# Kernel tuning notes

Measured on AMD Instinct MI355X. Metric: run time of the kernel, lower is better.

## Reference

```python
import jax, jax.numpy as jnp
import numpy as np

N, E, G = 50000, 800000, 64
F_IN, H = 128, 256


def setup_inputs() -> dict:
    key = jax.random.key(0)
    ks = jax.random.split(key, 16)
    s = 0.05
    return {
        "x": jax.random.normal(ks[0], (N, F_IN), jnp.float32),
        "edge_index": jax.random.randint(ks[1], (2, E), 0, N, jnp.int32),
        "batch": jnp.sort(jax.random.randint(ks[2], (N,), 0, G, jnp.int32)),
        "W1": jax.random.normal(ks[3], (F_IN, H), jnp.float32) * s,
        "b1": jnp.zeros((H,), jnp.float32),
        "W2": jax.random.normal(ks[4], (H, H), jnp.float32) * s,
        "b2": jnp.zeros((H,), jnp.float32),
        "W3": jax.random.normal(ks[5], (H, H), jnp.float32) * s,
        "b3": jnp.zeros((H,), jnp.float32),
        "Wc1": jax.random.normal(ks[6], (2 * H, 512), jnp.float32) * s,
        "bc1": jnp.zeros((512,), jnp.float32),
        "Wc2": jax.random.normal(ks[7], (512, 256), jnp.float32) * s,
        "bc2": jnp.zeros((256,), jnp.float32),
        "Wc3": jax.random.normal(ks[8], (256, 5), jnp.float32) * s,
        "bc3": jnp.zeros((5,), jnp.float32),
    }


def _gcn_conv(x, src, dst, dis, W, b):
    # PyG GCNConv: h = x W; out = D^{-1/2}(A+I)D^{-1/2} h + b
    h = x @ W                                        # [N, H]
    coef = (dis[src] * dis[dst])[:, None]            # [E, 1]
    agg = jax.ops.segment_sum(h[src] * coef, dst, num_segments=x.shape[0])
    return agg + h * (dis * dis)[:, None] + b        # self-loop term


def reference(x, edge_index, batch, W1, b1, W2, b2, W3, b3,
              Wc1, bc1, Wc2, bc2, Wc3, bc3):
    src, dst = edge_index[0], edge_index[1]
    # degree with self loops (in-degree at dst, as PyG)
    deg = jax.ops.segment_sum(jnp.ones_like(dst, jnp.float32), dst,
                              num_segments=x.shape[0]) + 1.0
    dis = jax.lax.rsqrt(deg)                         # D^{-1/2}

    h = jax.nn.relu(_gcn_conv(x, src, dst, dis, W1, b1))  # dropout=identity (eval)
    h = jax.nn.relu(_gcn_conv(h, src, dst, dis, W2, b2))
    h = jax.nn.relu(_gcn_conv(h, src, dst, dis, W3, b3))

    # global mean / max pool per graph
    cnt = jax.ops.segment_sum(jnp.ones_like(batch, jnp.float32), batch,
                              num_segments=G)
    x_mean = jax.ops.segment_sum(h, batch, num_segments=G) / jnp.maximum(cnt, 1.0)[:, None]
    x_max = jax.ops.segment_max(h, batch, num_segments=G)
    x_max = jnp.where(cnt[:, None] > 0, x_max, 0.0)  # guard empty segments
    g = jnp.concatenate([x_mean, x_max], axis=1)     # [G, 512]

    g = jax.nn.relu(g @ Wc1 + bc1)
    g = jax.nn.relu(g @ Wc2 + bc2)
    return g @ Wc3 + bc3                             # [G, 5]
```

## Files before the change

kernel.cpp:

```cpp
#include <hip/hip_runtime.h>
#include <cstdint>

#define CDIV(a, b) (((a) + (b) - 1) / (b))

typedef short bf16x8 __attribute__((ext_vector_type(8)));
typedef float f32x4 __attribute__((ext_vector_type(4)));

__device__ inline ushort f2bf_rn(float f) {
    uint32_t u = __float_as_uint(f);
    uint32_t rounding = 0x7FFF + ((u >> 16) & 1);
    return (ushort)((u + rounding) >> 16);
}
__device__ inline float bf2f(ushort h) { return __uint_as_float((uint32_t)h << 16); }

__global__ void k_init(int* __restrict__ degc, int N, float* __restrict__ sumbuf,
                       int* __restrict__ maxbuf, int PB) {
    int i = blockIdx.x * blockDim.x + threadIdx.x;
    if (i < N) degc[i] = 0;
    if (i < PB) { sumbuf[i] = 0.f; maxbuf[i] = 0; }
}

__global__ void k_deg(const int* __restrict__ dst, int E, int* __restrict__ degc) {
    int e = blockIdx.x * blockDim.x + threadIdx.x;
    if (e < E) atomicAdd(&degc[dst[e]], 1);
}

__global__ void k_xsplit(const float* __restrict__ x, int n, ushort* __restrict__ xhi) {
    int i = blockIdx.x * blockDim.x + threadIdx.x;
    if (i < n) xhi[i] = f2bf_rn(x[i]);
}

__global__ void k_scan_partial(const int* __restrict__ degc, int N, int* __restrict__ csum) {
    __shared__ int sm[256];
    int t = threadIdx.x;
    int idx = blockIdx.x * 1024 + t * 4;
    int s = 0;
#pragma unroll
    for (int j = 0; j < 4; ++j)
        if (idx + j < N) s += degc[idx + j];
    sm[t] = s;
    __syncthreads();
    for (int off = 128; off > 0; off >>= 1) {
        if (t < off) sm[t] += sm[t + off];
        __syncthreads();
    }
    if (t == 0) csum[blockIdx.x] = sm[0];
}

__global__ void k_scan_chunks(const int* __restrict__ csum, int nch, int* __restrict__ coff,
                              int* __restrict__ row_ptr, int N, int E) {
    if (threadIdx.x == 0 && blockIdx.x == 0) {
        int run = 0;
        for (int i = 0; i < nch; ++i) { coff[i] = run; run += csum[i]; }
        row_ptr[N] = E;
    }
}

__global__ void k_scan_final(const int* __restrict__ degc, int N, const int* __restrict__ coff,
                             int* __restrict__ row_ptr, int* __restrict__ fill,
                             float* __restrict__ dis) {
    __shared__ int sm[256];
    int t = threadIdx.x;
    int idx = blockIdx.x * 1024 + t * 4;
    int v[4];
    int s = 0;
#pragma unroll
    for (int j = 0; j < 4; ++j) {
        v[j] = (idx + j < N) ? degc[idx + j] : 0;
        s += v[j];
    }
    sm[t] = s;
    __syncthreads();
    for (int off = 1; off < 256; off <<= 1) {
        int x = (t >= off) ? sm[t - off] : 0;
        __syncthreads();
        sm[t] += x;
        __syncthreads();
    }
    int excl = sm[t] - s + coff[blockIdx.x];
#pragma unroll
    for (int j = 0; j < 4; ++j) {
        if (idx + j < N) {
            row_ptr[idx + j] = excl;
            fill[idx + j] = 0;
            dis[idx + j] = rsqrtf((float)v[j] + 1.0f);
            excl += v[j];
        }
    }
}

__global__ void k_fill(const int* __restrict__ src, const int* __restrict__ dst, int E,
                       const int* __restrict__ row_ptr, int* __restrict__ fill,
                       int* __restrict__ esrc) {
    int e = blockIdx.x * blockDim.x + threadIdx.x;
    if (e >= E) return;
    int d = dst[e], s = src[e];
    int pos = row_ptr[d] + atomicAdd(&fill[d], 1);
    esrc[pos] = s;
}

template <int C, bool SELF_F32>
__global__ __launch_bounds__(256) void k_agg(const float* __restrict__ xf,
                                             const ushort* __restrict__ hhi,
                                             const float* __restrict__ dis,
                                             const int* __restrict__ row_ptr,
                                             const int* __restrict__ esrc, int N,
                                             ushort* __restrict__ ohi,
                                             ushort* __restrict__ olo) {
    constexpr int V = C / 64;
    int wave = (blockIdx.x * blockDim.x + threadIdx.x) >> 6;
    int lane = threadIdx.x & 63;
    if (wave >= N) return;
    const int i = wave;
    const float di = dis[i];
    const float dd = di * di;
    float acc[V];
    if constexpr (SELF_F32) {
        const float* xr = xf + (size_t)i * C + lane * V;
        if constexpr (V == 4) {
            float4 v = *reinterpret_cast<const float4*>(xr);
            acc[0] = dd * v.x; acc[1] = dd * v.y; acc[2] = dd * v.z; acc[3] = dd * v.w;
        } else {
            float2 v = *reinterpret_cast<const float2*>(xr);
            acc[0] = dd * v.x; acc[1] = dd * v.y;
        }
    } else {
        size_t sb = (size_t)i * C + lane * V;
        if constexpr (V == 4) {
            ushort4 h = *reinterpret_cast<const ushort4*>(hhi + sb);
            acc[0] = dd * bf2f(h.x); acc[1] = dd * bf2f(h.y);
            acc[2] = dd * bf2f(h.z); acc[3] = dd * bf2f(h.w);
        } else {
            ushort2 h = *reinterpret_cast<const ushort2*>(hhi + sb);
            acc[0] = dd * bf2f(h.x); acc[1] = dd * bf2f(h.y);
        }
    }
    const int p0 = row_ptr[i], p1 = row_ptr[i + 1];
    int p = p0;
    if constexpr (V == 4) {
        for (; p + 4 <= p1; p += 4) {
            int s0 = esrc[p], s1 = esrc[p + 1], s2 = esrc[p + 2], s3 = esrc[p + 3];
            float c0 = dis[s0] * di, c1 = dis[s1] * di, c2 = dis[s2] * di, c3 = dis[s3] * di;
            ushort4 v0 = *reinterpret_cast<const ushort4*>(hhi + (size_t)s0 * C + lane * V);
            ushort4 v1 = *reinterpret_cast<const ushort4*>(hhi + (size_t)s1 * C + lane * V);
            ushort4 v2 = *reinterpret_cast<const ushort4*>(hhi + (size_t)s2 * C + lane * V);
            ushort4 v3 = *reinterpret_cast<const ushort4*>(hhi + (size_t)s3 * C + lane * V);
            acc[0] += c0 * bf2f(v0.x); acc[1] += c0 * bf2f(v0.y);
            acc[2] += c0 * bf2f(v0.z); acc[3] += c0 * bf2f(v0.w);
            acc[0] += c1 * bf2f(v1.x); acc[1] += c1 * bf2f(v1.y);
            acc[2] += c1 * bf2f(v1.z); acc[3] += c1 * bf2f(v1.w);
            acc[0] += c2 * bf2f(v2.x); acc[1] += c2 * bf2f(v2.y);
            acc[2] += c2 * bf2f(v2.z); acc[3] += c2 * bf2f(v2.w);
            acc[0] += c3 * bf2f(v3.x); acc[1] += c3 * bf2f(v3.y);
            acc[2] += c3 * bf2f(v3.z); acc[3] += c3 * bf2f(v3.w);
        }
        for (; p < p1; ++p) {
            int s = esrc[p];
            float c = dis[s] * di;
            ushort4 v = *reinterpret_cast<const ushort4*>(hhi + (size_t)s * C + lane * V);
            acc[0] += c * bf2f(v.x); acc[1] += c * bf2f(v.y);
            acc[2] += c * bf2f(v.z); acc[3] += c * bf2f(v.w);
        }
    } else {
        for (; p + 4 <= p1; p += 4) {
            int s0 = esrc[p], s1 = esrc[p + 1], s2 = esrc[p + 2], s3 = esrc[p + 3];
            float c0 = dis[s0] * di, c1 = dis[s1] * di, c2 = dis[s2] * di, c3 = dis[s3] * di;
            ushort2 v0 = *reinterpret_cast<const ushort2*>(hhi + (size_t)s0 * C + lane * V);
            ushort2 v1 = *reinterpret_cast<const ushort2*>(hhi + (size_t)s1 * C + lane * V);
            ushort2 v2 = *reinterpret_cast<const ushort2*>(hhi + (size_t)s2 * C + lane * V);
            ushort2 v3 = *reinterpret_cast<const ushort2*>(hhi + (size_t)s3 * C + lane * V);
            acc[0] += c0 * bf2f(v0.x); acc[1] += c0 * bf2f(v0.y);
            acc[0] += c1 * bf2f(v1.x); acc[1] += c1 * bf2f(v1.y);
            acc[0] += c2 * bf2f(v2.x); acc[1] += c2 * bf2f(v2.y);
            acc[0] += c3 * bf2f(v3.x); acc[1] += c3 * bf2f(v3.y);
        }
        for (; p < p1; ++p) {
            int s = esrc[p];
            float c = dis[s] * di;
            ushort2 v = *reinterpret_cast<const ushort2*>(hhi + (size_t)s * C + lane * V);
            acc[0] += c * bf2f(v.x); acc[1] += c * bf2f(v.y);
        }
    }
    ushort hi[V], lo[V];
#pragma unroll
    for (int j = 0; j < V; ++j) {
        hi[j] = f2bf_rn(acc[j]);
        lo[j] = f2bf_rn(acc[j] - bf2f(hi[j]));
    }
    const int c0 = lane * V;
    size_t fb = ((size_t)(i >> 4) * (C / 32) + (c0 >> 5)) * 512 +
                (size_t)(((i & 15) + ((c0 >> 3) & 3) * 16) * 8 + (c0 & 7));
    if constexpr (V == 4) {
        *reinterpret_cast<ushort4*>(ohi + fb) = make_ushort4(hi[0], hi[1], hi[2], hi[3]);
        *reinterpret_cast<ushort4*>(olo + fb) = make_ushort4(lo[0], lo[1], lo[2], lo[3]);
    } else {
        *reinterpret_cast<ushort2*>(ohi + fb) = make_ushort2(hi[0], hi[1]);
        *reinterpret_cast<ushort2*>(olo + fb) = make_ushort2(lo[0], lo[1]);
    }
}

__global__ void k_wsplit(const float* __restrict__ W, int K, ushort* __restrict__ Whi,
                         ushort* __restrict__ Wlo) {
    int idx = blockIdx.x * 256 + threadIdx.x;
    if (idx >= K * 256) return;
    int k = idx >> 8, n = idx & 255;
    float v = W[idx];
    ushort hi = f2bf_rn(v);
    ushort lo = f2bf_rn(v - bf2f(hi));
    int ks = k >> 5, r = k & 31;
    int lane = (r >> 3) * 16 + (n & 15);
    int j = r & 7;
    size_t d = (((size_t)ks * 16 + (n >> 4)) * 64 + lane) * 8 + j;
    Whi[d] = hi;
    Wlo[d] = lo;
}

template <int K, bool POOL>
__global__ __launch_bounds__(256) void k_gemm_bf16(const ushort* __restrict__ Ahi,
                                                   const ushort* __restrict__ Alo,
                                                   const ushort* __restrict__ Whi,
                                                   const ushort* __restrict__ Wlo,
                                                   const float* __restrict__ bias, int M,
                                                   ushort* __restrict__ Hhi,
                                                   const int* __restrict__ batch,
                                                   float* __restrict__ sumbuf,
                                                   int* __restrict__ maxbuf) {
    __shared__ ushort Bs[2][2][8][512];
    const int t = threadIdx.x;
    const int w = t >> 6, lane = t & 63;
    constexpr int KS = K / 32;

    const int nwg = (int)gridDim.x;
    const int orig = (int)blockIdx.x;
    const int q = nwg >> 3, r = nwg & 7;
    const int xcd = orig & 7;
    const int swz = (xcd < r ? xcd * (q + 1) : r * (q + 1) + (xcd - r) * q) + (orig >> 3);
    const int bm = (swz >> 1) * 128;
    const int bn = (swz & 1) * 128;
    const int rw = bm + w * 32;

    f32x4 acc[2][8] = {};

    const size_t fbase = ((size_t)(rw >> 4) * KS) * 512 + (size_t)lane * 8;
    const ushort* pa_h = Ahi + fbase;
    const ushort* pa_l = Alo + fbase;
    const size_t rb1 = (size_t)KS * 512;
    const int nf0 = bn >> 4;

    bf16x8 sbh[2], sbl[2];
    auto loadB = [&](int ks) {
#pragma unroll
        for (int q2 = 0; q2 < 2; ++q2) {
            int nf = (w << 1) | q2;
            size_t widx = (((size_t)ks * 16 + nf0 + nf) * 64 + lane) * 8;
            sbh[q2] = *reinterpret_cast<const bf16x8*>(Whi + widx);
            sbl[q2] = *reinterpret_cast<const bf16x8*>(Wlo + widx);
        }
    };
    auto writeB = [&](int b) {
#pragma unroll
        for (int q2 = 0; q2 < 2; ++q2) {
            int nf = (w << 1) | q2;
            *reinterpret_cast<bf16x8*>(&Bs[b][0][nf][lane * 8]) = sbh[q2];
            *reinterpret_cast<bf16x8*>(&Bs[b][1][nf][lane * 8]) = sbl[q2];
        }
    };

    bf16x8 c0h, c0l, c1h, c1l, n0h, n0l, n1h, n1l, m0h, m0l, m1h, m1l;
    auto loadA = [&](int ks, bf16x8& x0h, bf16x8& x0l, bf16x8& x1h, bf16x8& x1l) {
        size_t o = (size_t)ks * 512;
        x0h = *reinterpret_cast<const bf16x8*>(pa_h + o);
        x0l = *reinterpret_cast<const bf16x8*>(pa_l + o);
        x1h = *reinterpret_cast<const bf16x8*>(pa_h + rb1 + o);
        x1l = *reinterpret_cast<const bf16x8*>(pa_l + rb1 + o);
    };

    loadB(0);
    writeB(0);
    loadA(0, c0h, c0l, c1h, c1l);
    if (KS > 1) loadA(1, n0h, n0l, n1h, n1l);
    if (KS > 1) loadB(1);
    __syncthreads();

#pragma unroll
    for (int ks = 0; ks < KS; ++ks) {
        const int buf = ks & 1;
        if (ks + 2 < KS) loadA(ks + 2, m0h, m0l, m1h, m1l);
#pragma unroll
        for (int nf = 0; nf < 8; ++nf) {
            bf16x8 bh = *reinterpret_cast<const bf16x8*>(&Bs[buf][0][nf][lane * 8]);
            bf16x8 bl = *reinterpret_cast<const bf16x8*>(&Bs[buf][1][nf][lane * 8]);
            acc[0][nf] = __builtin_amdgcn_mfma_f32_16x16x32_bf16(c0h, bh, acc[0][nf], 0, 0, 0);
            acc[0][nf] = __builtin_amdgcn_mfma_f32_16x16x32_bf16(c0h, bl, acc[0][nf], 0, 0, 0);
            acc[0][nf] = __builtin_amdgcn_mfma_f32_16x16x32_bf16(c0l, bh, acc[0][nf], 0, 0, 0);
            acc[1][nf] = __builtin_amdgcn_mfma_f32_16x16x32_bf16(c1h, bh, acc[1][nf], 0, 0, 0);
            acc[1][nf] = __builtin_amdgcn_mfma_f32_16x16x32_bf16(c1h, bl, acc[1][nf], 0, 0, 0);
            acc[1][nf] = __builtin_amdgcn_mfma_f32_16x16x32_bf16(c1l, bh, acc[1][nf], 0, 0, 0);
        }
        if (ks + 1 < KS) {
            writeB(buf ^ 1);
            if (ks + 2 < KS) loadB(ks + 2);
            __syncthreads();
            c0h = n0h; c0l = n0l; c1h = n1h; c1l = n1l;
            n0h = m0h; n0l = m0l; n1h = m1h; n1l = m1l;
        }
    }

    const int colq = lane & 15;
    const int rowq = (lane >> 4) * 4;

    if constexpr (!POOL) {
#pragma unroll
        for (int m = 0; m < 2; ++m) {
#pragma unroll
            for (int nf = 0; nf < 8; ++nf) {
                int col = bn + nf * 16 + colq;
                float bia = bias[col];
#pragma unroll
                for (int r2 = 0; r2 < 4; ++r2) {
                    int rr = rw + m * 16 + rowq + r2;
                    if (rr < M) {
                        float v = fmaxf(acc[m][nf][r2] + bia, 0.f);
                        Hhi[(size_t)rr * 256 + col] = f2bf_rn(v);
                    }
                }
            }
        }
    } else {
        int r0 = min(rw + rowq, M - 1);
        int r7 = min(rw + 16 + rowq + 3, M - 1);
        int g0 = batch[r0];
        int g7 = batch[r7];
        int gfirst = __shfl(g0, 0);
        bool uni = __all(g0 == gfirst && g7 == gfirst);
        if (uni) {
#pragma unroll
            for (int nf = 0; nf < 8; ++nf) {
                int col = bn + nf * 16 + colq;
                float bia = bias[col];
                float s = 0.f, mx = 0.f;
#pragma unroll
                for (int m = 0; m < 2; ++m) {
#pragma unroll
                    for (int r2 = 0; r2 < 4; ++r2) {
                        int rr = rw + m * 16 + rowq + r2;
                        float v = fmaxf(acc[m][nf][r2] + bia, 0.f);
                        if (rr < M) { s += v; mx = fmaxf(mx, v); }
                    }
                }
                s += __shfl_xor(s, 16);
                mx = fmaxf(mx, __shfl_xor(mx, 16));
                s += __shfl_xor(s, 32);
                mx = fmaxf(mx, __shfl_xor(mx, 32));
                if ((lane >> 4) == 0) {
                    atomicAdd(&sumbuf[gfirst * 256 + col], s);
                    atomicMax(&maxbuf[gfirst * 256 + col], __float_as_int(mx));
                }
            }
        } else {
#pragma unroll
            for (int nf = 0; nf < 8; ++nf) {
                int col = bn + nf * 16 + colq;
                float bia = bias[col];
#pragma unroll
                for (int m = 0; m < 2; ++m) {
#pragma unroll
                    for (int r2 = 0; r2 < 4; ++r2) {
                        int rr = rw + m * 16 + rowq + r2;
                        if (rr < M) {
                            float v = fmaxf(acc[m][nf][r2] + bia, 0.f);
                            int g = batch[rr];
                            atomicAdd(&sumbuf[g * 256 + col], v);
                            atomicMax(&maxbuf[g * 256 + col], __float_as_int(v));
                        }
                    }
                }
            }
        }
    }
}

__global__ __launch_bounds__(512) void k_head(const float* __restrict__ sumbuf,
                                              const int* __restrict__ maxbuf,
                                              const int* __restrict__ batch, int N,
                                              const float* __restrict__ Wc1,
                                              const float* __restrict__ bc1,
                                              const float* __restrict__ Wc2,
                                              const float* __restrict__ bc2,
                                              const float* __restrict__ Wc3,
                                              const float* __restrict__ bc3,
                                              float* __restrict__ out) {
    __shared__ float gf[512];
    __shared__ float h1[512];
    __shared__ float h2[256];
    __shared__ int cntS;
    const int g = blockIdx.x;
    const int t = threadIdx.x;

    if (t == 0) {
        int lo = 0, hi = N;
        while (lo < hi) { int mid = (lo + hi) >> 1; if (batch[mid] < g) lo = mid + 1; else hi = mid; }
        int s = lo;
        lo = 0; hi = N;
        while (lo < hi) { int mid = (lo + hi) >> 1; if (batch[mid] < g + 1) lo = mid + 1; else hi = mid; }
        cntS = lo - s;
    }
    __syncthreads();
    const int cnt = cntS;
    if (t < 256) {
        float mean = sumbuf[g * 256 + t] / fmaxf((float)cnt, 1.0f);
        float mx = __int_as_float(maxbuf[g * 256 + t]);
        if (cnt == 0) { mean = 0.f; mx = 0.f; }
        gf[t] = mean;
        gf[256 + t] = mx;
    }
    __syncthreads();
    {
        float a0 = 0.f, a1 = 0.f, a2 = 0.f, a3 = 0.f;
        for (int k = 0; k < 512; k += 4) {
            a0 += gf[k + 0] * Wc1[(size_t)(k + 0) * 512 + t];
            a1 += gf[k + 1] * Wc1[(size_t)(k + 1) * 512 + t];
            a2 += gf[k + 2] * Wc1[(size_t)(k + 2) * 512 + t];
            a3 += gf[k + 3] * Wc1[(size_t)(k + 3) * 512 + t];
        }
        h1[t] = fmaxf((a0 + a1) + (a2 + a3) + bc1[t], 0.f);
    }
    __syncthreads();
    if (t < 256) {
        float a0 = 0.f, a1 = 0.f, a2 = 0.f, a3 = 0.f;
        for (int k = 0; k < 512; k += 4) {
            a0 += h1[k + 0] * Wc2[(size_t)(k + 0) * 256 + t];
            a1 += h1[k + 1] * Wc2[(size_t)(k + 1) * 256 + t];
            a2 += h1[k + 2] * Wc2[(size_t)(k + 2) * 256 + t];
            a3 += h1[k + 3] * Wc2[(size_t)(k + 3) * 256 + t];
        }
        h2[t] = fmaxf((a0 + a1) + (a2 + a3) + bc2[t], 0.f);
    }
    __syncthreads();
    if (t < 5) {
        float a = bc3[t];
        for (int k = 0; k < 256; ++k) a += h2[k] * Wc3[(size_t)k * 5 + t];
        out[(size_t)g * 5 + t] = a;
    }
}

extern "C" void kernel_launch(void* const* d_in, const int* in_sizes, int n_in, void* d_out,
                              int out_size, void* d_ws, size_t ws_size, hipStream_t stream) {
    const float* x = (const float*)d_in[0];
    const int* eidx = (const int*)d_in[1];
    const int* batch = (const int*)d_in[2];
    const float* W1 = (const float*)d_in[3];
    const float* b1 = (const float*)d_in[4];
    const float* W2 = (const float*)d_in[5];
    const float* b2 = (const float*)d_in[6];
    const float* W3 = (const float*)d_in[7];
    const float* b3 = (const float*)d_in[8];
    const float* Wc1 = (const float*)d_in[9];
    const float* bc1 = (const float*)d_in[10];
    const float* Wc2 = (const float*)d_in[11];
    const float* bc2 = (const float*)d_in[12];
    const float* Wc3 = (const float*)d_in[13];
    const float* bc3 = (const float*)d_in[14];
    float* out = (float*)d_out;

    const int N = in_sizes[2];
    const int E = in_sizes[1] / 2;
    const int G = out_size / 5;
    const int* src = eidx;
    const int* dst = eidx + E;
    const int Npad = CDIV(N, 128) * 128;

    char* p = (char*)d_ws;
    auto alloc = [&](size_t bytes) {
        void* r = (void*)p;
        p += (bytes + 255) & ~(size_t)255;
        return r;
    };
    float* dis = (float*)alloc((size_t)N * 4);
    int* degc = (int*)alloc((size_t)N * 4);
    int* row_ptr = (int*)alloc((size_t)(N + 1) * 4);
    int* fill = (int*)alloc((size_t)N * 4);
    const int nch = CDIV(N, 1024);
    int* csum = (int*)alloc((size_t)nch * 4);
    int* coff = (int*)alloc((size_t)nch * 4);
    int* esrc = (int*)alloc((size_t)E * 4);
    float* sumbuf = (float*)alloc((size_t)G * 256 * 4);
    int* maxbuf = (int*)alloc((size_t)G * 256 * 4);
    ushort* Ahi = (ushort*)alloc((size_t)Npad * 256 * 2);
    ushort* Alo = (ushort*)alloc((size_t)Npad * 256 * 2);
    ushort* Hhi = (ushort*)alloc((size_t)N * 256 * 2);
    ushort* Xhi = (ushort*)alloc((size_t)N * 128 * 2);
    ushort* W1hi = (ushort*)alloc((size_t)128 * 256 * 2);
    ushort* W1lo = (ushort*)alloc((size_t)128 * 256 * 2);
    ushort* W2hi = (ushort*)alloc((size_t)256 * 256 * 2);
    ushort* W2lo = (ushort*)alloc((size_t)256 * 256 * 2);
    ushort* W3hi = (ushort*)alloc((size_t)256 * 256 * 2);
    ushort* W3lo = (ushort*)alloc((size_t)256 * 256 * 2);
    (void)ws_size;

    k_init<<<CDIV(N, 256), 256, 0, stream>>>(degc, N, sumbuf, maxbuf, G * 256);

    k_wsplit<<<CDIV(128 * 256, 256), 256, 0, stream>>>(W1, 128, W1hi, W1lo);
    k_wsplit<<<CDIV(256 * 256, 256), 256, 0, stream>>>(W2, 256, W2hi, W2lo);
    k_wsplit<<<CDIV(256 * 256, 256), 256, 0, stream>>>(W3, 256, W3hi, W3lo);
    k_xsplit<<<CDIV(N * 128, 256), 256, 0, stream>>>(x, N * 128, Xhi);

    k_deg<<<CDIV(E, 256), 256, 0, stream>>>(dst, E, degc);
    k_scan_partial<<<nch, 256, 0, stream>>>(degc, N, csum);
    k_scan_chunks<<<1, 64, 0, stream>>>(csum, nch, coff, row_ptr, N, E);
    k_scan_final<<<nch, 256, 0, stream>>>(degc, N, coff, row_ptr, fill, dis);
    k_fill<<<CDIV(E, 256), 256, 0, stream>>>(src, dst, E, row_ptr, fill, esrc);

    const int ggrid = CDIV(N, 128) * 2;

    k_agg<128, true><<<CDIV(N * 64, 256), 256, 0, stream>>>(x, Xhi, dis, row_ptr, esrc, N,
                                                            Ahi, Alo);
    k_gemm_bf16<128, false><<<ggrid, 256, 0, stream>>>(Ahi, Alo, W1hi, W1lo, b1, N, Hhi,
                                                       batch, sumbuf, maxbuf);
    k_agg<256, false><<<CDIV(N * 64, 256), 256, 0, stream>>>(nullptr, Hhi, dis, row_ptr,
                                                             esrc, N, Ahi, Alo);
    k_gemm_bf16<256, false><<<ggrid, 256, 0, stream>>>(Ahi, Alo, W2hi, W2lo, b2, N, Hhi,
                                                       batch, sumbuf, maxbuf);
    k_agg<256, false><<<CDIV(N * 64, 256), 256, 0, stream>>>(nullptr, Hhi, dis, row_ptr,
                                                             esrc, N, Ahi, Alo);
    k_gemm_bf16<256, true><<<ggrid, 256, 0, stream>>>(Ahi, Alo, W3hi, W3lo, b3, N, Hhi,
                                                      batch, sumbuf, maxbuf);

    k_head<<<G, 512, 0, stream>>>(sumbuf, maxbuf, batch, N, Wc1, bc1, Wc2, bc2, Wc3, bc3, out);
}
```

Measured before the change: 453.3 us.

## Drop LDS staging for B, stream weights directly into registers; row-major A

The GEMM no longer stages weight fragments through double-buffered shared memory with barriers. Each wave now loads its pre-swizzled B fragments straight from global memory into register arrays, prefetching a few slots ahead. The aggregation kernel writes A in plain row-major order instead of fragment-tiled order, and the GEMM reads A rows with per-lane row clamping, so padded buffers are no longer needed. This removes LDS traffic and barriers, but each wave now fetches all eight B fragments itself, which multiplies global/L2 weight reads by four and raises register pressure. The row-major A reads are also less contiguous per lane.

```diff
diff --git a/kernel.cpp b/kernel.cpp
--- a/kernel.cpp
+++ b/kernel.cpp
@@ -187,15 +187,13 @@
         hi[j] = f2bf_rn(acc[j]);
         lo[j] = f2bf_rn(acc[j] - bf2f(hi[j]));
     }
-    const int c0 = lane * V;
-    size_t fb = ((size_t)(i >> 4) * (C / 32) + (c0 >> 5)) * 512 +
-                (size_t)(((i & 15) + ((c0 >> 3) & 3) * 16) * 8 + (c0 & 7));
+    size_t ob = (size_t)i * C + lane * V;
     if constexpr (V == 4) {
-        *reinterpret_cast<ushort4*>(ohi + fb) = make_ushort4(hi[0], hi[1], hi[2], hi[3]);
-        *reinterpret_cast<ushort4*>(olo + fb) = make_ushort4(lo[0], lo[1], lo[2], lo[3]);
+        *reinterpret_cast<ushort4*>(ohi + ob) = make_ushort4(hi[0], hi[1], hi[2], hi[3]);
+        *reinterpret_cast<ushort4*>(olo + ob) = make_ushort4(lo[0], lo[1], lo[2], lo[3]);
     } else {
-        *reinterpret_cast<ushort2*>(ohi + fb) = make_ushort2(hi[0], hi[1]);
-        *reinterpret_cast<ushort2*>(olo + fb) = make_ushort2(lo[0], lo[1]);
+        *reinterpret_cast<ushort2*>(ohi + ob) = make_ushort2(hi[0], hi[1]);
+        *reinterpret_cast<ushort2*>(olo + ob) = make_ushort2(lo[0], lo[1]);
     }
 }
 
@@ -225,10 +223,11 @@
                                                    const int* __restrict__ batch,
                                                    float* __restrict__ sumbuf,
                                                    int* __restrict__ maxbuf) {
-    __shared__ ushort Bs[2][2][8][512];
     const int t = threadIdx.x;
     const int w = t >> 6, lane = t & 63;
     constexpr int KS = K / 32;
+    constexpr int NSLOT = KS * 8;
+    constexpr int DB = 4;
 
     const int nwg = (int)gridDim.x;
     const int orig = (int)blockIdx.x;
@@ -241,69 +240,48 @@
 
     f32x4 acc[2][8] = {};
 
-    const size_t fbase = ((size_t)(rw >> 4) * KS) * 512 + (size_t)lane * 8;
-    const ushort* pa_h = Ahi + fbase;
-    const ushort* pa_l = Alo + fbase;
-    const size_t rb1 = (size_t)KS * 512;
+    int row0 = min(rw + (lane & 15), M - 1);
+    int row1 = min(rw + 16 + (lane & 15), M - 1);
+    const int kbase = (lane >> 4) * 8;
+    const ushort* pa0h = Ahi + (size_t)row0 * K + kbase;
+    const ushort* pa0l = Alo + (size_t)row0 * K + kbase;
+    const ushort* pa1h = Ahi + (size_t)row1 * K + kbase;
+    const ushort* pa1l = Alo + (size_t)row1 * K + kbase;
     const int nf0 = bn >> 4;
-
-    bf16x8 sbh[2], sbl[2];
-    auto loadB = [&](int ks) {
-#pragma unroll
-        for (int q2 = 0; q2 < 2; ++q2) {
-            int nf = (w << 1) | q2;
-            size_t widx = (((size_t)ks * 16 + nf0 + nf) * 64 + lane) * 8;
-            sbh[q2] = *reinterpret_cast<const bf16x8*>(Whi + widx);
-            sbl[q2] = *reinterpret_cast<const bf16x8*>(Wlo + widx);
-        }
+    const size_t wlanep = (size_t)lane * 8;
+
+    bf16x8 BH[NSLOT], BL[NSLOT];
+    bf16x8 AH0[KS], AL0[KS], AH1[KS], AL1[KS];
+
+    auto loadBslot = [&](int u) {
+        const int ks = u >> 3, nf = u & 7;
+        size_t widx = (((size_t)ks * 16 + nf0 + nf) * 64) * 8 + wlanep;
+        BH[u] = *reinterpret_cast<const bf16x8*>(Whi + widx);
+        BL[u] = *reinterpret_cast<const bf16x8*>(Wlo + widx);
     };
-    auto writeB = [&](int b) {
-#pragma unroll
-        for (int q2 = 0; q2 < 2; ++q2) {
-            int nf = (w << 1) | q2;
-            *reinterpret_cast<bf16x8*>(&Bs[b][0][nf][lane * 8]) = sbh[q2];
-            *reinterpret_cast<bf16x8*>(&Bs[b][1][nf][lane * 8]) = sbl[q2];
-        }
+    auto loadAset = [&](int ks) {
+        AH0[ks] = *reinterpret_cast<const bf16x8*>(pa0h + ks * 32);
+        AL0[ks] = *reinterpret_cast<const bf16x8*>(pa0l + ks * 32);
+        AH1[ks] = *reinterpret_cast<const bf16x8*>(pa1h + ks * 32);
+        AL1[ks] = *reinterpret_cast<const bf16x8*>(pa1l + ks * 32);
     };
 
-    bf16x8 c0h, c0l, c1h, c1l, n0h, n0l, n1h, n1l, m0h, m0l, m1h, m1l;
-    auto loadA = [&](int ks, bf16x8& x0h, bf16x8& x0l, bf16x8& x1h, bf16x8& x1l) {
-        size_t o = (size_t)ks * 512;
-        x0h = *reinterpret_cast<const bf16x8*>(pa_h + o);
-        x0l = *reinterpret_cast<const bf16x8*>(pa_l + o);
-        x1h = *reinterpret_cast<const bf16x8*>(pa_h + rb1 + o);
-        x1l = *reinterpret_cast<const bf16x8*>(pa_l + rb1 + o);
-    };
-
-    loadB(0);
-    writeB(0);
-    loadA(0, c0h, c0l, c1h, c1l);
-    if (KS > 1) loadA(1, n0h, n0l, n1h, n1l);
-    if (KS > 1) loadB(1);
-    __syncthreads();
-
-#pragma unroll
-    for (int ks = 0; ks < KS; ++ks) {
-        const int buf = ks & 1;
-        if (ks + 2 < KS) loadA(ks + 2, m0h, m0l, m1h, m1l);
-#pragma unroll
-        for (int nf = 0; nf < 8; ++nf) {
-            bf16x8 bh = *reinterpret_cast<const bf16x8*>(&Bs[buf][0][nf][lane * 8]);
-            bf16x8 bl = *reinterpret_cast<const bf16x8*>(&Bs[buf][1][nf][lane * 8]);
-            acc[0][nf] = __builtin_amdgcn_mfma_f32_16x16x32_bf16(c0h, bh, acc[0][nf], 0, 0, 0);
-            acc[0][nf] = __builtin_amdgcn_mfma_f32_16x16x32_bf16(c0h, bl, acc[0][nf], 0, 0, 0);
-            acc[0][nf] = __builtin_amdgcn_mfma_f32_16x16x32_bf16(c0l, bh, acc[0][nf], 0, 0, 0);
-            acc[1][nf] = __builtin_amdgcn_mfma_f32_16x16x32_bf16(c1h, bh, acc[1][nf], 0, 0, 0);
-            acc[1][nf] = __builtin_amdgcn_mfma_f32_16x16x32_bf16(c1h, bl, acc[1][nf], 0, 0, 0);
-            acc[1][nf] = __builtin_amdgcn_mfma_f32_16x16x32_bf16(c1l, bh, acc[1][nf], 0, 0, 0);
-        }
-        if (ks + 1 < KS) {
-            writeB(buf ^ 1);
-            if (ks + 2 < KS) loadB(ks + 2);
-            __syncthreads();
-            c0h = n0h; c0l = n0l; c1h = n1h; c1l = n1l;
-            n0h = m0h; n0l = m0l; n1h = m1h; n1l = m1l;
-        }
+#pragma unroll
+    for (int u = 0; u < DB; ++u) loadBslot(u);
+    loadAset(0);
+    if (KS > 1) loadAset(1);
+
+#pragma unroll
+    for (int u = 0; u < NSLOT; ++u) {
+        const int ks = u >> 3, nf = u & 7;
+        if (u + DB < NSLOT) loadBslot(u + DB);
+        if (nf == 0 && ks + 2 < KS) loadAset(ks + 2);
+        acc[0][nf] = __builtin_amdgcn_mfma_f32_16x16x32_bf16(AH0[ks], BH[u], acc[0][nf], 0, 0, 0);
+        acc[0][nf] = __builtin_amdgcn_mfma_f32_16x16x32_bf16(AH0[ks], BL[u], acc[0][nf], 0, 0, 0);
+        acc[0][nf] = __builtin_amdgcn_mfma_f32_16x16x32_bf16(AL0[ks], BH[u], acc[0][nf], 0, 0, 0);
+        acc[1][nf] = __builtin_amdgcn_mfma_f32_16x16x32_bf16(AH1[ks], BH[u], acc[1][nf], 0, 0, 0);
+        acc[1][nf] = __builtin_amdgcn_mfma_f32_16x16x32_bf16(AH1[ks], BL[u], acc[1][nf], 0, 0, 0);
+        acc[1][nf] = __builtin_amdgcn_mfma_f32_16x16x32_bf16(AL1[ks], BH[u], acc[1][nf], 0, 0, 0);
     }
 
     const int colq = lane & 15;
@@ -468,7 +446,6 @@
     const int G = out_size / 5;
     const int* src = eidx;
     const int* dst = eidx + E;
-    const int Npad = CDIV(N, 128) * 128;
 
     char* p = (char*)d_ws;
     auto alloc = [&](size_t bytes) {
@@ -486,8 +463,8 @@
     int* esrc = (int*)alloc((size_t)E * 4);
     float* sumbuf = (float*)alloc((size_t)G * 256 * 4);
     int* maxbuf = (int*)alloc((size_t)G * 256 * 4);
-    ushort* Ahi = (ushort*)alloc((size_t)Npad * 256 * 2);
-    ushort* Alo = (ushort*)alloc((size_t)Npad * 256 * 2);
+    ushort* Ahi = (ushort*)alloc((size_t)N * 256 * 2);
+    ushort* Alo = (ushort*)alloc((size_t)N * 256 * 2);
     ushort* Hhi = (ushort*)alloc((size_t)N * 256 * 2);
     ushort* Xhi = (ushort*)alloc((size_t)N * 128 * 2);
     ushort* W1hi = (ushort*)alloc((size_t)128 * 256 * 2);
```

Result: slower. 473.7 us (+4.5%).

## Use row-major A layout and 64-row GEMM tiles with one M-fragment per wave

Applied to the files above, without the earlier changes.

The aggregation kernel now writes its hi/lo bf16 outputs in plain row-major order instead of a pre-swizzled MFMA fragment layout. The GEMM reads A directly from row-major rows, with each lane loading 8 contiguous bf16. GEMM block tiles shrink from 128 to 64 rows, so each wave handles 16 rows, and the grid doubles. The intent is simpler, more coalesced scatter-free writes in aggregation and more GEMM blocks for occupancy. The cost is that the W fragments in LDS are reused over half as many rows, and the A loads become strided row reads.

```diff
diff --git a/kernel.cpp b/kernel.cpp
--- a/kernel.cpp
+++ b/kernel.cpp
@@ -187,15 +187,13 @@
         hi[j] = f2bf_rn(acc[j]);
         lo[j] = f2bf_rn(acc[j] - bf2f(hi[j]));
     }
-    const int c0 = lane * V;
-    size_t fb = ((size_t)(i >> 4) * (C / 32) + (c0 >> 5)) * 512 +
-                (size_t)(((i & 15) + ((c0 >> 3) & 3) * 16) * 8 + (c0 & 7));
+    size_t ob = (size_t)i * C + lane * V;
     if constexpr (V == 4) {
-        *reinterpret_cast<ushort4*>(ohi + fb) = make_ushort4(hi[0], hi[1], hi[2], hi[3]);
-        *reinterpret_cast<ushort4*>(olo + fb) = make_ushort4(lo[0], lo[1], lo[2], lo[3]);
+        *reinterpret_cast<ushort4*>(ohi + ob) = make_ushort4(hi[0], hi[1], hi[2], hi[3]);
+        *reinterpret_cast<ushort4*>(olo + ob) = make_ushort4(lo[0], lo[1], lo[2], lo[3]);
     } else {
-        *reinterpret_cast<ushort2*>(ohi + fb) = make_ushort2(hi[0], hi[1]);
-        *reinterpret_cast<ushort2*>(olo + fb) = make_ushort2(lo[0], lo[1]);
+        *reinterpret_cast<ushort2*>(ohi + ob) = make_ushort2(hi[0], hi[1]);
+        *reinterpret_cast<ushort2*>(olo + ob) = make_ushort2(lo[0], lo[1]);
     }
 }
 
@@ -235,16 +233,16 @@
     const int q = nwg >> 3, r = nwg & 7;
     const int xcd = orig & 7;
     const int swz = (xcd < r ? xcd * (q + 1) : r * (q + 1) + (xcd - r) * q) + (orig >> 3);
-    const int bm = (swz >> 1) * 128;
+    const int bm = (swz >> 1) * 64;
     const int bn = (swz & 1) * 128;
-    const int rw = bm + w * 32;
-
-    f32x4 acc[2][8] = {};
-
-    const size_t fbase = ((size_t)(rw >> 4) * KS) * 512 + (size_t)lane * 8;
-    const ushort* pa_h = Ahi + fbase;
-    const ushort* pa_l = Alo + fbase;
-    const size_t rb1 = (size_t)KS * 512;
+    const int rw = bm + w * 16;
+
+    f32x4 acc[8] = {};
+
+    int row0 = min(rw + (lane & 15), M - 1);
+    const int kbase = (lane >> 4) * 8;
+    const ushort* pa0h = Ahi + (size_t)row0 * K + kbase;
+    const ushort* pa0l = Alo + (size_t)row0 * K + kbase;
     const int nf0 = bn >> 4;
 
     bf16x8 sbh[2], sbl[2];
@@ -266,43 +264,37 @@
         }
     };
 
-    bf16x8 c0h, c0l, c1h, c1l, n0h, n0l, n1h, n1l, m0h, m0l, m1h, m1l;
-    auto loadA = [&](int ks, bf16x8& x0h, bf16x8& x0l, bf16x8& x1h, bf16x8& x1l) {
-        size_t o = (size_t)ks * 512;
-        x0h = *reinterpret_cast<const bf16x8*>(pa_h + o);
-        x0l = *reinterpret_cast<const bf16x8*>(pa_l + o);
-        x1h = *reinterpret_cast<const bf16x8*>(pa_h + rb1 + o);
-        x1l = *reinterpret_cast<const bf16x8*>(pa_l + rb1 + o);
+    bf16x8 c0h, c0l, n0h, n0l, m0h, m0l;
+    auto loadA = [&](int ks, bf16x8& xh, bf16x8& xl) {
+        xh = *reinterpret_cast<const bf16x8*>(pa0h + ks * 32);
+        xl = *reinterpret_cast<const bf16x8*>(pa0l + ks * 32);
     };
 
     loadB(0);
     writeB(0);
-    loadA(0, c0h, c0l, c1h, c1l);
-    if (KS > 1) loadA(1, n0h, n0l, n1h, n1l);
+    loadA(0, c0h, c0l);
+    if (KS > 1) loadA(1, n0h, n0l);
     if (KS > 1) loadB(1);
     __syncthreads();
 
 #pragma unroll
     for (int ks = 0; ks < KS; ++ks) {
         const int buf = ks & 1;
-        if (ks + 2 < KS) loadA(ks + 2, m0h, m0l, m1h, m1l);
+        if (ks + 2 < KS) loadA(ks + 2, m0h, m0l);
 #pragma unroll
         for (int nf = 0; nf < 8; ++nf) {
             bf16x8 bh = *reinterpret_cast<const bf16x8*>(&Bs[buf][0][nf][lane * 8]);
             bf16x8 bl = *reinterpret_cast<const bf16x8*>(&Bs[buf][1][nf][lane * 8]);
-            acc[0][nf] = __builtin_amdgcn_mfma_f32_16x16x32_bf16(c0h, bh, acc[0][nf], 0, 0, 0);
-            acc[0][nf] = __builtin_amdgcn_mfma_f32_16x16x32_bf16(c0h, bl, acc[0][nf], 0, 0, 0);
-            acc[0][nf] = __builtin_amdgcn_mfma_f32_16x16x32_bf16(c0l, bh, acc[0][nf], 0, 0, 0);
-            acc[1][nf] = __builtin_amdgcn_mfma_f32_16x16x32_bf16(c1h, bh, acc[1][nf], 0, 0, 0);
-            acc[1][nf] = __builtin_amdgcn_mfma_f32_16x16x32_bf16(c1h, bl, acc[1][nf], 0, 0, 0);
-            acc[1][nf] = __builtin_amdgcn_mfma_f32_16x16x32_bf16(c1l, bh, acc[1][nf], 0, 0, 0);
+            acc[nf] = __builtin_amdgcn_mfma_f32_16x16x32_bf16(c0h, bh, acc[nf], 0, 0, 0);
+            acc[nf] = __builtin_amdgcn_mfma_f32_16x16x32_bf16(c0h, bl, acc[nf], 0, 0, 0);
+            acc[nf] = __builtin_amdgcn_mfma_f32_16x16x32_bf16(c0l, bh, acc[nf], 0, 0, 0);
         }
         if (ks + 1 < KS) {
             writeB(buf ^ 1);
             if (ks + 2 < KS) loadB(ks + 2);
             __syncthreads();
-            c0h = n0h; c0l = n0l; c1h = n1h; c1l = n1l;
-            n0h = m0h; n0l = m0l; n1h = m1h; n1l = m1l;
+            c0h = n0h; c0l = n0l;
+            n0h = m0h; n0l = m0l;
         }
     }
 
@@ -311,28 +303,25 @@
 
     if constexpr (!POOL) {
 #pragma unroll
-        for (int m = 0; m < 2; ++m) {
-#pragma unroll
-            for (int nf = 0; nf < 8; ++nf) {
-                int col = bn + nf * 16 + colq;
-                float bia = bias[col];
-#pragma unroll
-                for (int r2 = 0; r2 < 4; ++r2) {
-                    int rr = rw + m * 16 + rowq + r2;
-                    if (rr < M) {
-                        float v = fmaxf(acc[m][nf][r2] + bia, 0.f);
-                        Hhi[(size_t)rr * 256 + col] = f2bf_rn(v);
-                    }
+        for (int nf = 0; nf < 8; ++nf) {
+            int col = bn + nf * 16 + colq;
+            float bia = bias[col];
+#pragma unroll
+            for (int r2 = 0; r2 < 4; ++r2) {
+                int rr = rw + rowq + r2;
+                if (rr < M) {
+                    float v = fmaxf(acc[nf][r2] + bia, 0.f);
+                    Hhi[(size_t)rr * 256 + col] = f2bf_rn(v);
                 }
             }
         }
     } else {
         int r0 = min(rw + rowq, M - 1);
-        int r7 = min(rw + 16 + rowq + 3, M - 1);
+        int r3 = min(rw + rowq + 3, M - 1);
         int g0 = batch[r0];
-        int g7 = batch[r7];
+        int g3 = batch[r3];
         int gfirst = __shfl(g0, 0);
-        bool uni = __all(g0 == gfirst && g7 == gfirst);
+        bool uni = __all(g0 == gfirst && g3 == gfirst);
         if (uni) {
 #pragma unroll
             for (int nf = 0; nf < 8; ++nf) {
@@ -340,13 +329,10 @@
                 float bia = bias[col];
                 float s = 0.f, mx = 0.f;
 #pragma unroll
-                for (int m = 0; m < 2; ++m) {
-#pragma unroll
-                    for (int r2 = 0; r2 < 4; ++r2) {
-                        int rr = rw + m * 16 + rowq + r2;
-                        float v = fmaxf(acc[m][nf][r2] + bia, 0.f);
-                        if (rr < M) { s += v; mx = fmaxf(mx, v); }
-                    }
+                for (int r2 = 0; r2 < 4; ++r2) {
+                    int rr = rw + rowq + r2;
+                    float v = fmaxf(acc[nf][r2] + bia, 0.f);
+                    if (rr < M) { s += v; mx = fmaxf(mx, v); }
                 }
                 s += __shfl_xor(s, 16);
                 mx = fmaxf(mx, __shfl_xor(mx, 16));
@@ -363,16 +349,13 @@
                 int col = bn + nf * 16 + colq;
                 float bia = bias[col];
 #pragma unroll
-                for (int m = 0; m < 2; ++m) {
-#pragma unroll
-                    for (int r2 = 0; r2 < 4; ++r2) {
-                        int rr = rw + m * 16 + rowq + r2;
-                        if (rr < M) {
-                            float v = fmaxf(acc[m][nf][r2] + bia, 0.f);
-                            int g = batch[rr];
-                            atomicAdd(&sumbuf[g * 256 + col], v);
-                            atomicMax(&maxbuf[g * 256 + col], __float_as_int(v));
-                        }
+                for (int r2 = 0; r2 < 4; ++r2) {
+                    int rr = rw + rowq + r2;
+                    if (rr < M) {
+                        float v = fmaxf(acc[nf][r2] + bia, 0.f);
+                        int g = batch[rr];
+                        atomicAdd(&sumbuf[g * 256 + col], v);
+                        atomicMax(&maxbuf[g * 256 + col], __float_as_int(v));
                     }
                 }
             }
@@ -468,7 +451,6 @@
     const int G = out_size / 5;
     const int* src = eidx;
     const int* dst = eidx + E;
-    const int Npad = CDIV(N, 128) * 128;
 
     char* p = (char*)d_ws;
     auto alloc = [&](size_t bytes) {
@@ -486,8 +468,8 @@
     int* esrc = (int*)alloc((size_t)E * 4);
     float* sumbuf = (float*)alloc((size_t)G * 256 * 4);
     int* maxbuf = (int*)alloc((size_t)G * 256 * 4);
-    ushort* Ahi = (ushort*)alloc((size_t)Npad * 256 * 2);
-    ushort* Alo = (ushort*)alloc((size_t)Npad * 256 * 2);
+    ushort* Ahi = (ushort*)alloc((size_t)N * 256 * 2);
+    ushort* Alo = (ushort*)alloc((size_t)N * 256 * 2);
     ushort* Hhi = (ushort*)alloc((size_t)N * 256 * 2);
     ushort* Xhi = (ushort*)alloc((size_t)N * 128 * 2);
     ushort* W1hi = (ushort*)alloc((size_t)128 * 256 * 2);
@@ -511,7 +493,7 @@
     k_scan_final<<<nch, 256, 0, stream>>>(degc, N, coff, row_ptr, fill, dis);
     k_fill<<<CDIV(E, 256), 256, 0, stream>>>(src, dst, E, row_ptr, fill, esrc);
 
-    const int ggrid = CDIV(N, 128) * 2;
+    const int ggrid = CDIV(N, 64) * 2;
 
     k_agg<128, true><<<CDIV(N * 64, 256), 256, 0, stream>>>(x, Xhi, dis, row_ptr, esrc, N,
                                                             Ahi, Alo);
```

After: 418.6 us (median of 2 runs). 1.08x faster.
